# Optimization experiments

Hardware: AMD Instinct MI355X
Metric: run time of the kernel (lower is better)

## Reference

```python
import jax, jax.numpy as jnp
import numpy as np

N_HEADS = 8
TANH_CLIP = 10.0
NEG = -1e9  # finite stand-in for -inf so log_softmax/vjp stay NaN-free


def setup_inputs() -> dict:
    key = jax.random.key(0)
    ks = jax.random.split(key, 8)
    B, N, D = 256, 1000, 128
    embeddings = jax.random.normal(ks[0], (B, N, D), dtype=jnp.float32)
    W_node = jax.random.normal(ks[1], (D, 3 * D), dtype=jnp.float32) * (1.0 / np.sqrt(D))
    W_fixed = jax.random.normal(ks[2], (D, D), dtype=jnp.float32) * (1.0 / np.sqrt(D))
    W_step = jax.random.normal(ks[3], (2 * D, D), dtype=jnp.float32) * (1.0 / np.sqrt(2 * D))
    W_out = jax.random.normal(ks[4], (D, D), dtype=jnp.float32) * (1.0 / np.sqrt(D))
    first_idx = jax.random.randint(ks[5], (B,), 0, N)
    last_idx = jax.random.randint(ks[6], (B,), 0, N)
    mask = jax.random.randint(ks[7], (B, N), 0, 2).astype(jnp.bool_)
    mask = mask.at[:, 0].set(False)  # guarantee at least one feasible node
    return {"embeddings": embeddings, "W_node": W_node, "W_fixed": W_fixed,
            "W_step": W_step, "W_out": W_out, "first_idx": first_idx,
            "last_idx": last_idx, "mask": mask}


def reference(embeddings, W_node, W_fixed, W_step, W_out, first_idx, last_idx, mask):
    # One pointer-network decode step (TSP variant of AttentionModel._get_log_p),
    # including the _precompute projections.
    B, N, D = embeddings.shape
    H = N_HEADS
    dk = D // H

    # _precompute: fixed context + glimpse K/V + logit key
    graph_embed = embeddings.mean(axis=1)                       # [B, D]
    fixed_ctx = graph_embed @ W_fixed                           # [B, D]
    kvl = embeddings @ W_node                                   # [B, N, 3D]
    K, V, logit_K = jnp.split(kvl, 3, axis=-1)                  # each [B, N, D]

    # step context: cat(first-node emb, last-node emb) -> project to D
    b = jnp.arange(B)
    step_ctx = jnp.concatenate([embeddings[b, first_idx], embeddings[b, last_idx]], axis=-1)  # [B, 2D]
    q = fixed_ctx + step_ctx @ W_step                           # [B, D]

    # masked multi-head glimpse attention (q_len = 1)
    qh = q.reshape(B, H, dk)                                    # [B, H, dk]
    Kh = K.reshape(B, N, H, dk)
    Vh = V.reshape(B, N, H, dk)
    compat = jnp.einsum('bhd,bnhd->bhn', qh, Kh) / np.sqrt(dk)  # [B, H, N]
    compat = jnp.where(mask[:, None, :], NEG, compat)           # mask_inner
    attn = jax.nn.softmax(compat, axis=-1)
    heads = jnp.einsum('bhn,bnhd->bhd', attn, Vh)               # [B, H, dk]
    glimpse = heads.reshape(B, D) @ W_out                       # [B, D]

    # single-head logit attention with tanh clipping
    logits = jnp.einsum('bd,bnd->bn', glimpse, logit_K) / np.sqrt(D)  # [B, N]
    logits = jnp.tanh(logits) * TANH_CLIP
    logits = jnp.where(mask, NEG, logits)                       # mask_logits
    return jax.nn.log_softmax(logits, axis=-1)                  # [B, N]
```

## Files before the change

kernel.cpp:

```cpp
#include <hip/hip_runtime.h>


#define NEG (-1e9f)

__global__ void k_detect(const uint4* __restrict__ mw, int* __restrict__ flag)
{
    __shared__ int any_s;
    if (threadIdx.x == 0) any_s = 0;
    __syncthreads();
    unsigned acc = 0;
    #pragma unroll
    for (int i = 0; i < 4; ++i) {
        const uint4 v = mw[i * 256 + threadIdx.x];
        acc |= (v.x | v.y | v.z | v.w) & 0xFFFFFF00u;
    }
    if (acc) atomicOr(&any_s, 1);
    __syncthreads();
    if (threadIdx.x == 0) *flag = any_s;
}

__global__ __launch_bounds__(1024) void k_pre(
    const float* __restrict__ E, const float* __restrict__ Wn,
    const float* __restrict__ Wf, const float* __restrict__ Ws,
    const int* __restrict__ fi, const int* __restrict__ li,
    float* __restrict__ qkp)
{
    const int b = blockIdx.x;
    const int t = threadIdx.x;
    __shared__ float4 red4[1024];
    __shared__ float mu[128], e1[128], e2[128], q[128];
    __shared__ float qred[8][128];

    const float4* E4 = (const float4*)(E + (size_t)b * 128000);

    {
        const int c4 = t & 31, s = t >> 5;
        float4 acc = make_float4(0.f, 0.f, 0.f, 0.f);
        for (int r = s; r < 1000; r += 32) {
            float4 v = E4[r * 32 + c4];
            acc.x += v.x; acc.y += v.y; acc.z += v.z; acc.w += v.w;
        }
        red4[t] = acc;
    }
    if (t >= 512 && t < 544) {
        ((float4*)e1)[t - 512] = E4[fi[b] * 32 + (t - 512)];
    } else if (t >= 544 && t < 576) {
        ((float4*)e2)[t - 544] = E4[li[b] * 32 + (t - 544)];
    }
    __syncthreads();
    if (t < 32) {
        float4 acc = red4[t];
        #pragma unroll
        for (int s = 1; s < 32; ++s) {
            float4 v = red4[s * 32 + t];
            acc.x += v.x; acc.y += v.y; acc.z += v.z; acc.w += v.w;
        }
        const float inv = 1.0f / 1000.0f;
        ((float4*)mu)[t] = make_float4(acc.x * inv, acc.y * inv, acc.z * inv, acc.w * inv);
    }
    __syncthreads();
    {
        const int part = t >> 7, d = t & 127;
        float acc = 0.f;
        const int k0 = part * 48;
        for (int k = k0; k < k0 + 48; ++k) {
            const float s = (k < 128) ? mu[k] : (k < 256 ? e1[k - 128] : e2[k - 256]);
            const float w = (k < 128) ? Wf[k * 128 + d] : Ws[(k - 128) * 128 + d];
            acc += s * w;
        }
        qred[part][d] = acc;
    }
    __syncthreads();
    if (t < 128) {
        float acc = 0.f;
        #pragma unroll
        for (int p = 0; p < 8; ++p) acc += qred[p][t];
        q[t] = acc;
    }
    __syncthreads();
    {
        const int j = t & 127, cg = t >> 7;
        const float qj = q[j];
        for (int c0 = 0; c0 < 128; c0 += 8) {
            const int c = c0 + cg;
            float v = Wn[c * 384 + j] * qj;
            v += __shfl_down(v, 8, 16);
            v += __shfl_down(v, 4, 16);
            v += __shfl_down(v, 2, 16);
            v += __shfl_down(v, 1, 16);
            if ((j & 15) == 0) qkp[b * 1024 + (j >> 4) * 128 + c] = v * 0.25f;
        }
    }
}

__global__ __launch_bounds__(512) void k_glimpse(
    const float* __restrict__ E, const float* __restrict__ Wn,
    const float* __restrict__ Wo,
    const int* __restrict__ maskI, const unsigned char* __restrict__ maskB,
    const int* __restrict__ flag,
    const float* __restrict__ qkp, float* __restrict__ glp)
{
    const int b = blockIdx.x;
    const int t = threadIdx.x;
    __shared__ float4 qk4[256];
    __shared__ float4 Et[4096];
    __shared__ float pc[128 * 36];
    __shared__ float ct[128 * 9];
    __shared__ float pt[128 * 8];
    __shared__ float redh[8 * 9];
    __shared__ float mh[8], lh[8], al[8];
    __shared__ float EbarF[8 * 128];
    __shared__ float heads[128];
    __shared__ float gl[128];

    const float4* E4 = (const float4*)(E + (size_t)b * 128000);
    const bool useB = (*flag != 0);

    if (t < 256) {
        const int h = t >> 5, g = t & 31;
        qk4[h * 32 + (g ^ (g >> 3))] = ((const float4*)(qkp + b * 1024))[t];
    }
    if (t < 8) { mh[t] = -3e38f; lh[t] = 0.f; }
    float4 eacc[8];
    #pragma unroll
    for (int h = 0; h < 8; ++h) eacc[h] = make_float4(0.f, 0.f, 0.f, 0.f);
    const int c4 = t & 31, sl = t >> 5;
    const int rr = t >> 2, qq = t & 3;
    __syncthreads();

    for (int tile = 0; tile < 8; ++tile) {
        const int r0 = tile * 128;
        {
            const int g = r0 + rr;
            float4 v[8];
            if (g < 1000) {
                #pragma unroll
                for (int i = 0; i < 8; ++i) v[i] = E4[g * 32 + qq * 8 + i];
            } else {
                #pragma unroll
                for (int i = 0; i < 8; ++i) v[i] = make_float4(0.f, 0.f, 0.f, 0.f);
            }
            float pch[8];
            #pragma unroll
            for (int h = 0; h < 8; ++h) pch[h] = 0.f;
            #pragma unroll
            for (int i = 0; i < 8; ++i) {
                const int grp = qq * 8 + i;
                Et[rr * 32 + (grp ^ (rr & 7))] = v[i];
                #pragma unroll
                for (int h = 0; h < 8; ++h) {
                    float4 w = qk4[h * 32 + (grp ^ qq)];
                    pch[h] += v[i].x * w.x + v[i].y * w.y + v[i].z * w.z + v[i].w * w.w;
                }
            }
            #pragma unroll
            for (int h = 0; h < 8; ++h) pc[rr * 36 + qq * 9 + h] = pch[h];
        }
        __syncthreads();
        #pragma unroll
        for (int k = 0; k < 2; ++k) {
            const int idx = t + k * 512;
            const int row = idx >> 3, h = idx & 7;
            float s = pc[row * 36 + h] + pc[row * 36 + 9 + h]
                    + pc[row * 36 + 18 + h] + pc[row * 36 + 27 + h];
            const int g = r0 + row;
            const bool m = (g >= 1000) ||
                (useB ? (maskB[b * 1000 + g] != 0) : (maskI[b * 1000 + g] != 0));
            ct[row * 9 + h] = m ? NEG : s;
        }
        __syncthreads();
        if (t < 64) {
            const int h = t & 7, part = t >> 3;
            float mt = -3e38f;
            const int rb = part * 16;
            for (int r = 0; r < 16; ++r) mt = fmaxf(mt, ct[(rb + r) * 9 + h]);
            redh[part * 9 + h] = mt;
        }
        __syncthreads();
        if (t < 8) {
            float mt = redh[t];
            for (int p = 1; p < 8; ++p) mt = fmaxf(mt, redh[p * 9 + t]);
            const float mnew = fmaxf(mh[t], mt);
            al[t] = __expf(mh[t] - mnew);
            mh[t] = mnew;
        }
        __syncthreads();
        #pragma unroll
        for (int k = 0; k < 2; ++k) {
            const int idx = t + k * 512;
            const int row = idx >> 3, h = idx & 7;
            pt[row * 8 + h] = __expf(ct[row * 9 + h] - mh[h]);
        }
        __syncthreads();
        {
            #pragma unroll
            for (int h = 0; h < 8; ++h) {
                const float a = al[h];
                eacc[h].x *= a; eacc[h].y *= a; eacc[h].z *= a; eacc[h].w *= a;
            }
            #pragma unroll
            for (int j = 0; j < 8; ++j) {
                const int r = sl * 8 + j;
                const float4 ev = Et[r * 32 + (c4 ^ (r & 7))];
                const float4 p0 = ((float4*)pt)[r * 2];
                const float4 p1 = ((float4*)pt)[r * 2 + 1];
                eacc[0].x += p0.x * ev.x; eacc[0].y += p0.x * ev.y; eacc[0].z += p0.x * ev.z; eacc[0].w += p0.x * ev.w;
                eacc[1].x += p0.y * ev.x; eacc[1].y += p0.y * ev.y; eacc[1].z += p0.y * ev.z; eacc[1].w += p0.y * ev.w;
                eacc[2].x += p0.z * ev.x; eacc[2].y += p0.z * ev.y; eacc[2].z += p0.z * ev.z; eacc[2].w += p0.z * ev.w;
                eacc[3].x += p0.w * ev.x; eacc[3].y += p0.w * ev.y; eacc[3].z += p0.w * ev.z; eacc[3].w += p0.w * ev.w;
                eacc[4].x += p1.x * ev.x; eacc[4].y += p1.x * ev.y; eacc[4].z += p1.x * ev.z; eacc[4].w += p1.x * ev.w;
                eacc[5].x += p1.y * ev.x; eacc[5].y += p1.y * ev.y; eacc[5].z += p1.y * ev.z; eacc[5].w += p1.y * ev.w;
                eacc[6].x += p1.z * ev.x; eacc[6].y += p1.z * ev.y; eacc[6].z += p1.z * ev.z; eacc[6].w += p1.z * ev.w;
                eacc[7].x += p1.w * ev.x; eacc[7].y += p1.w * ev.y; eacc[7].z += p1.w * ev.z; eacc[7].w += p1.w * ev.w;
            }
        }
        if (t < 64) {
            const int h = t & 7, part = t >> 3;
            float s = 0.f;
            const int rb = part * 16;
            for (int r = 0; r < 16; ++r) s += pt[(rb + r) * 8 + h];
            redh[part * 9 + h] = s;
        }
        __syncthreads();
        if (t < 8) {
            float s = 0.f;
            for (int p = 0; p < 8; ++p) s += redh[p * 9 + t];
            lh[t] = lh[t] * al[t] + s;
        }
    }

    #pragma unroll
    for (int h = 0; h < 8; ++h) Et[sl * 256 + h * 32 + c4] = eacc[h];
    __syncthreads();
    if (t < 256) {
        const int h = t >> 5, cc = t & 31;
        float4 s = make_float4(0.f, 0.f, 0.f, 0.f);
        #pragma unroll
        for (int s2 = 0; s2 < 16; ++s2) {
            float4 v = Et[s2 * 256 + h * 32 + cc];
            s.x += v.x; s.y += v.y; s.z += v.z; s.w += v.w;
        }
        const float invl = 1.0f / lh[h];
        ((float4*)EbarF)[h * 32 + cc] =
            make_float4(s.x * invl, s.y * invl, s.z * invl, s.w * invl);
    }
    __syncthreads();
    if (t < 128) {
        const int h = t >> 4;
        float acc = 0.f;
        for (int c = 0; c < 128; ++c) acc += EbarF[h * 128 + c] * Wn[c * 384 + 128 + t];
        heads[t] = acc;
    }
    __syncthreads();
    if (t < 128) {
        float acc = 0.f;
        for (int j2 = 0; j2 < 128; ++j2) acc += heads[j2] * Wo[j2 * 128 + t];
        gl[t] = acc;
    }
    __syncthreads();
    if (t < 128) {
        float acc = 0.f;
        for (int d2 = 0; d2 < 128; ++d2) acc += Wn[t * 384 + 256 + d2] * gl[d2];
        glp[b * 128 + t] = acc * 0.08838834764831845f;
    }
}

__global__ __launch_bounds__(1024) void k_logits(
    const float* __restrict__ E,
    const int* __restrict__ maskI, const unsigned char* __restrict__ maskB,
    const int* __restrict__ flag,
    const float* __restrict__ glp, float* __restrict__ out)
{
    const int b = blockIdx.x;
    const int t = threadIdx.x;
    __shared__ float gl[128];
    __shared__ float z[1024];
    __shared__ float pc[128 * 9];
    __shared__ float red[16];
    __shared__ float stat[2];

    const float4* E4 = (const float4*)(E + (size_t)b * 128000);
    const bool useB = (*flag != 0);
    if (t < 32) ((float4*)gl)[t] = ((const float4*)(glp + b * 128))[t];
    __syncthreads();

    const int row = t >> 3, sub = t & 7;
    for (int tile = 0; tile < 8; ++tile) {
        const int g = tile * 128 + row;
        float acc = 0.f;
        if (g < 1000) {
            #pragma unroll
            for (int i = 0; i < 4; ++i) {
                const float4 v = E4[g * 32 + sub * 4 + i];
                const float4 w = ((float4*)gl)[sub * 4 + i];
                acc += v.x * w.x + v.y * w.y + v.z * w.z + v.w * w.w;
            }
        }
        pc[row * 9 + sub] = acc;
        __syncthreads();
        if (t < 128) {
            const int g2 = tile * 128 + t;
            if (g2 < 1000) {
                float s = 0.f;
                #pragma unroll
                for (int q2 = 0; q2 < 8; ++q2) s += pc[t * 9 + q2];
                float zz = 10.0f * tanhf(s);
                const bool m = useB ? (maskB[b * 1000 + g2] != 0)
                                    : (maskI[b * 1000 + g2] != 0);
                if (m) zz = NEG;
                z[g2] = zz;
            }
        }
        __syncthreads();
    }
    float v = (t < 1000) ? z[t] : -3e38f;
    #pragma unroll
    for (int off = 32; off > 0; off >>= 1) v = fmaxf(v, __shfl_down(v, off, 64));
    if ((t & 63) == 0) red[t >> 6] = v;
    __syncthreads();
    if (t == 0) {
        float m = red[0];
        for (int i = 1; i < 16; ++i) m = fmaxf(m, red[i]);
        stat[0] = m;
    }
    __syncthreads();
    const float zmax = stat[0];
    float sv = (t < 1000) ? __expf(z[t] - zmax) : 0.f;
    #pragma unroll
    for (int off = 32; off > 0; off >>= 1) sv += __shfl_down(sv, off, 64);
    if ((t & 63) == 0) red[t >> 6] = sv;
    __syncthreads();
    if (t == 0) {
        float s = 0.f;
        for (int i = 0; i < 16; ++i) s += red[i];
        stat[1] = zmax + __logf(s);
    }
    __syncthreads();
    if (t < 1000)
        out[(size_t)b * 1000 + t] = z[t] - stat[1];
}

extern "C" void kernel_launch(void* const* d_in, const int* in_sizes, int n_in,
                              void* d_out, int out_size, void* d_ws, size_t ws_size,
                              hipStream_t stream) {
    const float* E  = (const float*)d_in[0];
    const float* Wn = (const float*)d_in[1];
    const float* Wf = (const float*)d_in[2];
    const float* Ws = (const float*)d_in[3];
    const float* Wo = (const float*)d_in[4];
    const int*   fi = (const int*)d_in[5];
    const int*   li = (const int*)d_in[6];
    const int*   maskI = (const int*)d_in[7];
    const unsigned char* maskB = (const unsigned char*)d_in[7];
    float* out = (float*)d_out;

    float* qkp = (float*)d_ws;
    float* glp = qkp + 256 * 1024;
    int*   flag = (int*)(glp + 256 * 128);

    k_detect<<<1, 256, 0, stream>>>((const uint4*)d_in[7], flag);
    k_pre<<<256, 1024, 0, stream>>>(E, Wn, Wf, Ws, fi, li, qkp);
    k_glimpse<<<256, 512, 0, stream>>>(E, Wn, Wo, maskI, maskB, flag, qkp, glp);
    k_logits<<<256, 1024, 0, stream>>>(E, maskI, maskB, flag, glp, out);
}
```

Before: 299.6 us.

## Fuse detect, precompute, glimpse and logits kernels into one per-batch kernel

Result: faster. 281.8 us (-5.9%).

```diff
diff --git a/kernel.cpp b/kernel.cpp
--- a/kernel.cpp
+++ b/kernel.cpp
@@ -3,62 +3,73 @@
 
 #define NEG (-1e9f)
 
-__global__ void k_detect(const uint4* __restrict__ mw, int* __restrict__ flag)
-{
-    __shared__ int any_s;
-    if (threadIdx.x == 0) any_s = 0;
-    __syncthreads();
-    unsigned acc = 0;
-    #pragma unroll
-    for (int i = 0; i < 4; ++i) {
-        const uint4 v = mw[i * 256 + threadIdx.x];
-        acc |= (v.x | v.y | v.z | v.w) & 0xFFFFFF00u;
-    }
-    if (acc) atomicOr(&any_s, 1);
-    __syncthreads();
-    if (threadIdx.x == 0) *flag = any_s;
-}
-
-__global__ __launch_bounds__(1024) void k_pre(
+__global__ __launch_bounds__(1024) void k_fused(
     const float* __restrict__ E, const float* __restrict__ Wn,
     const float* __restrict__ Wf, const float* __restrict__ Ws,
+    const float* __restrict__ Wo,
     const int* __restrict__ fi, const int* __restrict__ li,
-    float* __restrict__ qkp)
+    const int* __restrict__ maskI, const unsigned char* __restrict__ maskB,
+    float* __restrict__ out)
 {
     const int b = blockIdx.x;
     const int t = threadIdx.x;
-    __shared__ float4 red4[1024];
-    __shared__ float mu[128], e1[128], e2[128], q[128];
+
+    __shared__ float4 Et[4096];
+    __shared__ float4 qk4[256];
+    __shared__ float4 pt4[256];
+    __shared__ float4 EbarF4[256];
+    __shared__ float4 mu4[32], e14[32], e24[32], gp4[32];
+    __shared__ float q[128], heads[128], gl[128];
     __shared__ float qred[8][128];
+    __shared__ float ct[128 * 9];
+    __shared__ float redh[72];
+    __shared__ float mh[8], lh[8], al[8];
+    __shared__ float red[16];
+    __shared__ float stat[2];
+    __shared__ int flagS;
+
+    float* const mu = (float*)mu4;
+    float* const e1 = (float*)e14;
+    float* const e2 = (float*)e24;
+    float* const gp = (float*)gp4;
+    float* const pt = (float*)pt4;
+    float* const EbarF = (float*)EbarF4;
+    float* const qkf = (float*)qk4;
 
     const float4* E4 = (const float4*)(E + (size_t)b * 128000);
 
-    {
-        const int c4 = t & 31, s = t >> 5;
+    if (t == 0) flagS = 0;
+    const uint4 dv = ((const uint4*)maskI)[t];
+    const unsigned det = (dv.x | dv.y | dv.z | dv.w) & 0xFFFFFF00u;
+
+    {
+        const int cm = t & 31, sm = t >> 5;
         float4 acc = make_float4(0.f, 0.f, 0.f, 0.f);
-        for (int r = s; r < 1000; r += 32) {
-            float4 v = E4[r * 32 + c4];
+        for (int r = sm; r < 1000; r += 32) {
+            const float4 v = E4[r * 32 + cm];
             acc.x += v.x; acc.y += v.y; acc.z += v.z; acc.w += v.w;
         }
-        red4[t] = acc;
+        Et[t] = acc;
     }
     if (t >= 512 && t < 544) {
-        ((float4*)e1)[t - 512] = E4[fi[b] * 32 + (t - 512)];
+        e14[t - 512] = E4[fi[b] * 32 + (t - 512)];
     } else if (t >= 544 && t < 576) {
-        ((float4*)e2)[t - 544] = E4[li[b] * 32 + (t - 544)];
-    }
-    __syncthreads();
+        e24[t - 544] = E4[li[b] * 32 + (t - 544)];
+    }
+    __syncthreads();
+    if (det) atomicOr(&flagS, 1);
     if (t < 32) {
-        float4 acc = red4[t];
+        float4 acc = Et[t];
         #pragma unroll
         for (int s = 1; s < 32; ++s) {
-            float4 v = red4[s * 32 + t];
+            const float4 v = Et[s * 32 + t];
             acc.x += v.x; acc.y += v.y; acc.z += v.z; acc.w += v.w;
         }
         const float inv = 1.0f / 1000.0f;
-        ((float4*)mu)[t] = make_float4(acc.x * inv, acc.y * inv, acc.z * inv, acc.w * inv);
-    }
-    __syncthreads();
+        mu4[t] = make_float4(acc.x * inv, acc.y * inv, acc.z * inv, acc.w * inv);
+    }
+    __syncthreads();
+
     {
         const int part = t >> 7, d = t & 127;
         float acc = 0.f;
@@ -88,85 +99,58 @@
             v += __shfl_down(v, 4, 16);
             v += __shfl_down(v, 2, 16);
             v += __shfl_down(v, 1, 16);
-            if ((j & 15) == 0) qkp[b * 1024 + (j >> 4) * 128 + c] = v * 0.25f;
-        }
-    }
-}
-
-__global__ __launch_bounds__(512) void k_glimpse(
-    const float* __restrict__ E, const float* __restrict__ Wn,
-    const float* __restrict__ Wo,
-    const int* __restrict__ maskI, const unsigned char* __restrict__ maskB,
-    const int* __restrict__ flag,
-    const float* __restrict__ qkp, float* __restrict__ glp)
-{
-    const int b = blockIdx.x;
-    const int t = threadIdx.x;
-    __shared__ float4 qk4[256];
-    __shared__ float4 Et[4096];
-    __shared__ float pc[128 * 36];
-    __shared__ float ct[128 * 9];
-    __shared__ float pt[128 * 8];
-    __shared__ float redh[8 * 9];
-    __shared__ float mh[8], lh[8], al[8];
-    __shared__ float EbarF[8 * 128];
-    __shared__ float heads[128];
-    __shared__ float gl[128];
-
-    const float4* E4 = (const float4*)(E + (size_t)b * 128000);
-    const bool useB = (*flag != 0);
-
-    if (t < 256) {
-        const int h = t >> 5, g = t & 31;
-        qk4[h * 32 + (g ^ (g >> 3))] = ((const float4*)(qkp + b * 1024))[t];
-    }
+            if ((j & 15) == 0) {
+                const int h = j >> 4, s = c >> 2;
+                qkf[h * 128 + (s ^ (s >> 2)) * 4 + (c & 3)] = v * 0.25f;
+            }
+        }
+    }
+    __syncthreads();
+
+    const bool useB = (flagS != 0);
+
     if (t < 8) { mh[t] = -3e38f; lh[t] = 0.f; }
     float4 eacc[8];
     #pragma unroll
     for (int h = 0; h < 8; ++h) eacc[h] = make_float4(0.f, 0.f, 0.f, 0.f);
     const int c4 = t & 31, sl = t >> 5;
-    const int rr = t >> 2, qq = t & 3;
-    __syncthreads();
+    const int rr = t >> 3, qq = t & 7;
 
     for (int tile = 0; tile < 8; ++tile) {
         const int r0 = tile * 128;
         {
             const int g = r0 + rr;
-            float4 v[8];
+            float4 v[4];
             if (g < 1000) {
                 #pragma unroll
-                for (int i = 0; i < 8; ++i) v[i] = E4[g * 32 + qq * 8 + i];
+                for (int i = 0; i < 4; ++i) v[i] = E4[g * 32 + qq * 4 + i];
             } else {
                 #pragma unroll
-                for (int i = 0; i < 8; ++i) v[i] = make_float4(0.f, 0.f, 0.f, 0.f);
+                for (int i = 0; i < 4; ++i) v[i] = make_float4(0.f, 0.f, 0.f, 0.f);
             }
             float pch[8];
             #pragma unroll
             for (int h = 0; h < 8; ++h) pch[h] = 0.f;
             #pragma unroll
-            for (int i = 0; i < 8; ++i) {
-                const int grp = qq * 8 + i;
+            for (int i = 0; i < 4; ++i) {
+                const int grp = qq * 4 + i;
                 Et[rr * 32 + (grp ^ (rr & 7))] = v[i];
+                const int sg = grp ^ (grp >> 2);
                 #pragma unroll
                 for (int h = 0; h < 8; ++h) {
-                    float4 w = qk4[h * 32 + (grp ^ qq)];
+                    const float4 w = qk4[h * 32 + sg];
                     pch[h] += v[i].x * w.x + v[i].y * w.y + v[i].z * w.z + v[i].w * w.w;
                 }
             }
             #pragma unroll
-            for (int h = 0; h < 8; ++h) pc[rr * 36 + qq * 9 + h] = pch[h];
-        }
-        __syncthreads();
-        #pragma unroll
-        for (int k = 0; k < 2; ++k) {
-            const int idx = t + k * 512;
-            const int row = idx >> 3, h = idx & 7;
-            float s = pc[row * 36 + h] + pc[row * 36 + 9 + h]
-                    + pc[row * 36 + 18 + h] + pc[row * 36 + 27 + h];
-            const int g = r0 + row;
-            const bool m = (g >= 1000) ||
-                (useB ? (maskB[b * 1000 + g] != 0) : (maskI[b * 1000 + g] != 0));
-            ct[row * 9 + h] = m ? NEG : s;
+            for (int m = 1; m <= 4; m <<= 1) {
+                #pragma unroll
+                for (int h = 0; h < 8; ++h) pch[h] += __shfl_xor(pch[h], m, 64);
+            }
+            bool msk = (g >= 1000);
+            if (!msk) msk = useB ? (maskB[b * 1000 + g] != 0)
+                                 : (maskI[b * 1000 + g] != 0);
+            ct[rr * 9 + qq] = msk ? NEG : pch[qq];
         }
         __syncthreads();
         if (t < 64) {
@@ -185,10 +169,8 @@
             mh[t] = mnew;
         }
         __syncthreads();
-        #pragma unroll
-        for (int k = 0; k < 2; ++k) {
-            const int idx = t + k * 512;
-            const int row = idx >> 3, h = idx & 7;
+        {
+            const int row = t >> 3, h = t & 7;
             pt[row * 8 + h] = __expf(ct[row * 9 + h] - mh[h]);
         }
         __syncthreads();
@@ -199,11 +181,11 @@
                 eacc[h].x *= a; eacc[h].y *= a; eacc[h].z *= a; eacc[h].w *= a;
             }
             #pragma unroll
-            for (int j = 0; j < 8; ++j) {
-                const int r = sl * 8 + j;
+            for (int j = 0; j < 4; ++j) {
+                const int r = sl * 4 + j;
                 const float4 ev = Et[r * 32 + (c4 ^ (r & 7))];
-                const float4 p0 = ((float4*)pt)[r * 2];
-                const float4 p1 = ((float4*)pt)[r * 2 + 1];
+                const float4 p0 = pt4[r * 2];
+                const float4 p1 = pt4[r * 2 + 1];
                 eacc[0].x += p0.x * ev.x; eacc[0].y += p0.x * ev.y; eacc[0].z += p0.x * ev.z; eacc[0].w += p0.x * ev.w;
                 eacc[1].x += p0.y * ev.x; eacc[1].y += p0.y * ev.y; eacc[1].z += p0.y * ev.z; eacc[1].w += p0.y * ev.w;
                 eacc[2].x += p0.z * ev.x; eacc[2].y += p0.z * ev.y; eacc[2].z += p0.z * ev.z; eacc[2].w += p0.z * ev.w;
@@ -229,91 +211,111 @@
         }
     }
 
-    #pragma unroll
-    for (int h = 0; h < 8; ++h) Et[sl * 256 + h * 32 + c4] = eacc[h];
+    if (sl >= 16) {
+        #pragma unroll
+        for (int h = 0; h < 8; ++h) Et[(sl - 16) * 256 + h * 32 + c4] = eacc[h];
+    }
+    __syncthreads();
+    if (sl < 16) {
+        #pragma unroll
+        for (int h = 0; h < 8; ++h) {
+            const float4 o = Et[sl * 256 + h * 32 + c4];
+            eacc[h].x += o.x; eacc[h].y += o.y; eacc[h].z += o.z; eacc[h].w += o.w;
+            Et[sl * 256 + h * 32 + c4] = eacc[h];
+        }
+    }
     __syncthreads();
     if (t < 256) {
         const int h = t >> 5, cc = t & 31;
         float4 s = make_float4(0.f, 0.f, 0.f, 0.f);
         #pragma unroll
         for (int s2 = 0; s2 < 16; ++s2) {
-            float4 v = Et[s2 * 256 + h * 32 + cc];
+            const float4 v = Et[s2 * 256 + h * 32 + cc];
             s.x += v.x; s.y += v.y; s.z += v.z; s.w += v.w;
         }
         const float invl = 1.0f / lh[h];
-        ((float4*)EbarF)[h * 32 + cc] =
-            make_float4(s.x * invl, s.y * invl, s.z * invl, s.w * invl);
+        EbarF4[h * 32 + cc] = make_float4(s.x * invl, s.y * invl, s.z * invl, s.w * invl);
+    }
+    __syncthreads();
+
+    {
+        const int part = t >> 7, d = t & 127, h = d >> 4;
+        float acc = 0.f;
+        const int c0 = part * 16;
+        for (int c = c0; c < c0 + 16; ++c) acc += EbarF[h * 128 + c] * Wn[c * 384 + 128 + d];
+        qred[part][d] = acc;
     }
     __syncthreads();
     if (t < 128) {
-        const int h = t >> 4;
-        float acc = 0.f;
-        for (int c = 0; c < 128; ++c) acc += EbarF[h * 128 + c] * Wn[c * 384 + 128 + t];
+        float acc = 0.f;
+        #pragma unroll
+        for (int p = 0; p < 8; ++p) acc += qred[p][t];
         heads[t] = acc;
     }
     __syncthreads();
+    {
+        const int part = t >> 7, d = t & 127;
+        float acc = 0.f;
+        const int j0 = part * 16;
+        for (int j = j0; j < j0 + 16; ++j) acc += heads[j] * Wo[j * 128 + d];
+        qred[part][d] = acc;
+    }
+    __syncthreads();
     if (t < 128) {
         float acc = 0.f;
-        for (int j2 = 0; j2 < 128; ++j2) acc += heads[j2] * Wo[j2 * 128 + t];
+        #pragma unroll
+        for (int p = 0; p < 8; ++p) acc += qred[p][t];
         gl[t] = acc;
     }
     __syncthreads();
+    {
+        const int part = t >> 7, c = t & 127;
+        float acc = 0.f;
+        const int d0 = part * 16;
+        for (int d = d0; d < d0 + 16; ++d) acc += Wn[c * 384 + 256 + d] * gl[d];
+        qred[part][c] = acc;
+    }
+    __syncthreads();
     if (t < 128) {
         float acc = 0.f;
-        for (int d2 = 0; d2 < 128; ++d2) acc += Wn[t * 384 + 256 + d2] * gl[d2];
-        glp[b * 128 + t] = acc * 0.08838834764831845f;
-    }
-}
-
-__global__ __launch_bounds__(1024) void k_logits(
-    const float* __restrict__ E,
-    const int* __restrict__ maskI, const unsigned char* __restrict__ maskB,
-    const int* __restrict__ flag,
-    const float* __restrict__ glp, float* __restrict__ out)
-{
-    const int b = blockIdx.x;
-    const int t = threadIdx.x;
-    __shared__ float gl[128];
-    __shared__ float z[1024];
-    __shared__ float pc[128 * 9];
-    __shared__ float red[16];
-    __shared__ float stat[2];
-
-    const float4* E4 = (const float4*)(E + (size_t)b * 128000);
-    const bool useB = (*flag != 0);
-    if (t < 32) ((float4*)gl)[t] = ((const float4*)(glp + b * 128))[t];
-    __syncthreads();
-
-    const int row = t >> 3, sub = t & 7;
-    for (int tile = 0; tile < 8; ++tile) {
-        const int g = tile * 128 + row;
-        float acc = 0.f;
-        if (g < 1000) {
-            #pragma unroll
-            for (int i = 0; i < 4; ++i) {
-                const float4 v = E4[g * 32 + sub * 4 + i];
-                const float4 w = ((float4*)gl)[sub * 4 + i];
-                acc += v.x * w.x + v.y * w.y + v.z * w.z + v.w * w.w;
-            }
-        }
-        pc[row * 9 + sub] = acc;
-        __syncthreads();
-        if (t < 128) {
-            const int g2 = tile * 128 + t;
-            if (g2 < 1000) {
-                float s = 0.f;
-                #pragma unroll
-                for (int q2 = 0; q2 < 8; ++q2) s += pc[t * 9 + q2];
-                float zz = 10.0f * tanhf(s);
-                const bool m = useB ? (maskB[b * 1000 + g2] != 0)
-                                    : (maskI[b * 1000 + g2] != 0);
-                if (m) zz = NEG;
-                z[g2] = zz;
-            }
-        }
-        __syncthreads();
-    }
-    float v = (t < 1000) ? z[t] : -3e38f;
+        #pragma unroll
+        for (int p = 0; p < 8; ++p) acc += qred[p][t];
+        gp[t] = acc * 0.08838834764831845f;
+    }
+    __syncthreads();
+
+    {
+        const int row = t >> 3, sub = t & 7;
+        for (int tile = 0; tile < 8; ++tile) {
+            const int g = tile * 128 + row;
+            float acc = 0.f;
+            if (g < 1000) {
+                #pragma unroll
+                for (int i = 0; i < 4; ++i) {
+                    const float4 v = E4[g * 32 + sub * 4 + i];
+                    const float4 w = gp4[sub * 4 + i];
+                    acc += v.x * w.x + v.y * w.y + v.z * w.z + v.w * w.w;
+                }
+            }
+            ct[row * 9 + sub] = acc;
+            __syncthreads();
+            if (t < 128) {
+                const int g2 = tile * 128 + t;
+                if (g2 < 1000) {
+                    float s = 0.f;
+                    #pragma unroll
+                    for (int k = 0; k < 8; ++k) s += ct[t * 9 + k];
+                    float zz = 10.0f * tanhf(s);
+                    const bool m = useB ? (maskB[b * 1000 + g2] != 0)
+                                        : (maskI[b * 1000 + g2] != 0);
+                    if (m) zz = NEG;
+                    pt[g2] = zz;
+                }
+            }
+            __syncthreads();
+        }
+    }
+    float v = (t < 1000) ? pt[t] : -3e38f;
     #pragma unroll
     for (int off = 32; off > 0; off >>= 1) v = fmaxf(v, __shfl_down(v, off, 64));
     if ((t & 63) == 0) red[t >> 6] = v;
@@ -324,8 +326,7 @@
         stat[0] = m;
     }
     __syncthreads();
-    const float zmax = stat[0];
-    float sv = (t < 1000) ? __expf(z[t] - zmax) : 0.f;
+    float sv = (t < 1000) ? __expf(pt[t] - stat[0]) : 0.f;
     #pragma unroll
     for (int off = 32; off > 0; off >>= 1) sv += __shfl_down(sv, off, 64);
     if ((t & 63) == 0) red[t >> 6] = sv;
@@ -333,11 +334,11 @@
     if (t == 0) {
         float s = 0.f;
         for (int i = 0; i < 16; ++i) s += red[i];
-        stat[1] = zmax + __logf(s);
+        stat[1] = stat[0] + __logf(s);
     }
     __syncthreads();
     if (t < 1000)
-        out[(size_t)b * 1000 + t] = z[t] - stat[1];
+        out[(size_t)b * 1000 + t] = pt[t] - stat[1];
 }
 
 extern "C" void kernel_launch(void* const* d_in, const int* in_sizes, int n_in,
@@ -354,12 +355,5 @@
     const unsigned char* maskB = (const unsigned char*)d_in[7];
     float* out = (float*)d_out;
 
-    float* qkp = (float*)d_ws;
-    float* glp = qkp + 256 * 1024;
-    int*   flag = (int*)(glp + 256 * 128);
-
-    k_detect<<<1, 256, 0, stream>>>((const uint4*)d_in[7], flag);
-    k_pre<<<256, 1024, 0, stream>>>(E, Wn, Wf, Ws, fi, li, qkp);
-    k_glimpse<<<256, 512, 0, stream>>>(E, Wn, Wo, maskI, maskB, flag, qkp, glp);
-    k_logits<<<256, 1024, 0, stream>>>(E, maskI, maskB, flag, glp, out);
+    k_fused<<<256, 1024, 0, stream>>>(E, Wn, Wf, Ws, Wo, fi, li, maskI, maskB, out);
 }
```
